# Kernel optimization log

Measured on AMD Instinct MI355X. Metric: run time of the kernel, lower is better.

Reference implementation:

```python
import jax, jax.numpy as jnp
import numpy as np

L = 256
C = 20
B = 4096


def _pairwise_mask(L, C):
    # mask[l1, c1, l2, c2] = (l2 - l1 >= 1), independent of c1, c2
    ls = np.arange(L)
    m = (ls[None, :] - ls[:, None]) >= 1            # (L, L)
    mask = np.broadcast_to(m[:, None, :, None], (L, C, L, C))
    return jnp.asarray(mask[None], dtype=bool)       # (1, L, C, L, C)


def setup_inputs() -> dict:
    key = jax.random.key(0)
    k1, k2, k3, k4 = jax.random.split(key, 4)
    # one-hot sequences, flattened to (B, L*C) like the layer's input
    seq = jax.random.randint(k1, (B, L), 0, C)
    x_lc = jax.nn.one_hot(seq, C, dtype=jnp.float32).reshape(B, L * C)
    theta_0 = jax.random.normal(k2, (1,), dtype=jnp.float32)
    theta_lc = (jax.random.normal(k3, (1, L, C), dtype=jnp.float32)
                / np.sqrt(L).astype(np.float32))
    mask = _pairwise_mask(L, C)
    theta_lclc = (jax.random.normal(k4, (1, L, C, L, C), dtype=jnp.float32)
                  / np.float32(L)) * mask
    return {"x_lc": x_lc, "theta_0": theta_0, "theta_lc": theta_lc,
            "theta_lclc": theta_lclc, "mask": mask}


def reference(x_lc, theta_0, theta_lc, theta_lclc, mask):
    # x_lc: (B, L*C); reshape to (B, L, C)
    x = x_lc.reshape(-1, L, C)
    # additive term: sum over (l, c)
    phi = theta_0 + jnp.einsum('blc,lc->b', x, theta_lc[0])[:, None]  # (B, 1)
    # masked pairwise quadratic form: x^T (theta * mask) x, computed as a
    # GEMM instead of materializing the (B, L, C, L, C) broadcast tensor.
    Theta = (theta_lclc[0] * mask[0].astype(theta_lclc.dtype)).reshape(L * C, L * C)
    xf = x_lc  # (B, L*C)
    quad = jnp.sum((xf @ Theta) * xf, axis=1, keepdims=True)  # (B, 1)
    return phi + quad
```

## Files before the change

### kernel.cpp

```cpp
#include <hip/hip_runtime.h>

#define LPOS 256
#define CCH 20
#define BB 4096
#define LC 5120


__global__ __launch_bounds__(256) void k_prepare(
    const float* __restrict__ x_lc, const float* __restrict__ theta_0,
    const float* __restrict__ theta_lc, unsigned char* __restrict__ seqC,
    float* __restrict__ out)
{
    const int b = blockIdx.x;
    const int l = threadIdx.x;
    const float* xp = x_lc + (size_t)b * LC + (size_t)l * CCH;
    const float4* xp4 = reinterpret_cast<const float4*>(xp);
    float v[CCH];
#pragma unroll
    for (int q = 0; q < 5; ++q) {
        float4 t = xp4[q];
        v[q * 4 + 0] = t.x; v[q * 4 + 1] = t.y;
        v[q * 4 + 2] = t.z; v[q * 4 + 3] = t.w;
    }
    int s = 0; float best = v[0];
#pragma unroll
    for (int c = 1; c < CCH; ++c) { if (v[c] > best) { best = v[c]; s = c; } }

    seqC[((size_t)(l >> 3) * BB + b) * 8 + (l & 7)] = (unsigned char)s;

    float lin = theta_lc[l * CCH + s];
#pragma unroll
    for (int off = 32; off > 0; off >>= 1) lin += __shfl_down(lin, off, 64);
    __shared__ float partial[4];
    const int wave = threadIdx.x >> 6;
    const int lane = threadIdx.x & 63;
    if (lane == 0) partial[wave] = lin;
    __syncthreads();
    if (threadIdx.x == 0)
        out[b] = theta_0[0] + partial[0] + partial[1] + partial[2] + partial[3];
}

#define QT 512
#define NC 8
#define NMC 32
#define NQUADS 800
#define SEGS 13
#define TBLP (SEGS * 256)

template <int MODE>
__global__ __launch_bounds__(QT, 8) void k_quad(
    const float* __restrict__ Theta,
    const uint2* __restrict__ seqC,
    float* __restrict__ part,
    float* __restrict__ out)
{
    __shared__ float Tl[TBLP];

    const int c   = blockIdx.x;
    const int g   = blockIdx.y;
    const int tid = threadIdx.x;
    const int wave = tid >> 6;
    const int lane = tid & 63;

    const int l1arr[2] = { g, 254 - g };
    const int m0a = (g + 1) >> 3;
    const int m0b = (255 - g) >> 3;
    const int n1 = NMC - m0a;
    const int L  = (g == 127) ? n1 : n1 + (NMC - m0b);

    int base[2][8];
#pragma unroll
    for (int q = 0; q < 2; ++q) {
        const int l1 = l1arr[q];
        const int mw = l1 >> 3;
        const int wsel = (l1 >> 2) & 1;
        const int sh = (l1 & 3) * 8;
#pragma unroll
        for (int i = 0; i < 8; ++i) {
            const uint2 u = seqC[(size_t)mw * BB + i * QT + tid];
            const unsigned w = wsel ? u.y : u.x;
            base[q][i] = (int)((w >> sh) & 0xFFu) * CCH;
        }
    }

    float acc[8];
#pragma unroll
    for (int i = 0; i < 8; ++i) acc[i] = 0.f;

    for (int t = c; t < L; t += NC) {
        int l1, m, jl, rq;
        if (t < n1) { rq = 0; l1 = l1arr[0]; m = m0a + t;
                      jl = (t == 0) ? ((l1 + 1) & 7) : 0; }
        else        { rq = 1; l1 = l1arr[1]; m = m0b + (t - n1);
                      jl = (t == n1) ? ((l1 + 1) & 7) : 0; }

        __syncthreads();
#pragma unroll
        for (int k = 0; k < 2; ++k) {
            const int seg = wave + 8 * k;
            if (seg < SEGS) {
                const int u0 = seg * 64 + lane;
                const int u = (u0 < NQUADS) ? u0 : (NQUADS - 1);
                const int r = u / 5, cc = u - r * 5;
                const int j = r / CCH, s1 = r - j * CCH;
                const float* gp = Theta + (size_t)(l1 * CCH + s1) * LC
                                        + (m * 8 + j) * CCH + cc * 4;
                float* lp = Tl + seg * 256;
                __builtin_amdgcn_global_load_lds(
                    (const __attribute__((address_space(1))) void*)gp,
                    (__attribute__((address_space(3))) void*)lp, 16, 0, 0);
            }
        }
        __syncthreads();

        if (jl == 0) {
#pragma unroll
            for (int i = 0; i < 8; ++i) {
                const uint2 u = seqC[(size_t)m * BB + i * QT + tid];
#pragma unroll
                for (int j = 0; j < 8; ++j) {
                    const unsigned w = (j < 4) ? u.x : u.y;
                    const int s2 = (w >> ((j & 3) * 8)) & 0xFF;
                    acc[i] += Tl[j * 400 + base[rq][i] + s2];
                }
            }
        } else {
#pragma unroll
            for (int i = 0; i < 8; ++i) {
                const uint2 u = seqC[(size_t)m * BB + i * QT + tid];
#pragma unroll
                for (int j = 0; j < 8; ++j) {
                    const unsigned w = (j < 4) ? u.x : u.y;
                    const int s2 = (w >> ((j & 3) * 8)) & 0xFF;
                    const float v = Tl[j * 400 + base[rq][i] + s2];
                    acc[i] += (j >= jl) ? v : 0.f;
                }
            }
        }
    }

    if (MODE == 0) {
        float* row = part + (size_t)(c * 128 + g) * BB;
#pragma unroll
        for (int i = 0; i < 8; ++i) row[i * QT + tid] = acc[i];
    } else {
#pragma unroll
        for (int i = 0; i < 8; ++i) atomicAdd(&out[i * QT + tid], acc[i]);
    }
}

__global__ __launch_bounds__(256) void k_reduce(
    const float4* __restrict__ part4,
    float* __restrict__ out)
{
    const int b4 = blockIdx.x * 256 + threadIdx.x;
    const int r0 = blockIdx.y * 128;
    float4 a = make_float4(0.f, 0.f, 0.f, 0.f);
    for (int r = r0; r < r0 + 128; ++r) {
        const float4 p = part4[(size_t)r * 1024 + b4];
        a.x += p.x; a.y += p.y; a.z += p.z; a.w += p.w;
    }
    atomicAdd(&out[b4 * 4 + 0], a.x);
    atomicAdd(&out[b4 * 4 + 1], a.y);
    atomicAdd(&out[b4 * 4 + 2], a.z);
    atomicAdd(&out[b4 * 4 + 3], a.w);
}

extern "C" void kernel_launch(void* const* d_in, const int* in_sizes, int n_in,
                              void* d_out, int out_size, void* d_ws, size_t ws_size,
                              hipStream_t stream) {
    const float* x_lc       = (const float*)d_in[0];
    const float* theta_0    = (const float*)d_in[1];
    const float* theta_lc   = (const float*)d_in[2];
    const float* theta_lclc = (const float*)d_in[3];
    float* out = (float*)d_out;

    unsigned char* seqC = (unsigned char*)d_ws;
    float* part = (float*)((char*)d_ws + (1 << 20));
    const size_t need = (1 << 20) + (size_t)1024 * BB * 4;

    k_prepare<<<dim3(BB), dim3(256), 0, stream>>>(x_lc, theta_0, theta_lc, seqC, out);
    if (ws_size >= need) {
        k_quad<0><<<dim3(NC, 128), dim3(QT), 0, stream>>>(
            theta_lclc, (const uint2*)seqC, part, out);
        k_reduce<<<dim3(4, 8), dim3(256), 0, stream>>>(
            (const float4*)part, out);
    } else {
        k_quad<1><<<dim3(NC, 128), dim3(QT), 0, stream>>>(
            theta_lclc, (const uint2*)seqC, part, out);
    }
}
```

Baseline: 68.80 us.

## Flatten quad work into 4-chunk blocks with double-buffered LDS staging

Replaces the 8x128 grid, where each block walks a strided list of (l1, m) chunks, with a flat grid of 1048 blocks that each process four consecutive chunks. Theta tiles are double-buffered in LDS so the next chunk's global_load_lds runs while the current one is consumed. The sequence words and base indices for the next chunk are prefetched into registers. This doubles LDS use per block, which may lower occupancy, and grows the partial buffer and reduction to 1048 rows.

After: 248.9 us. 262% more time.

```diff
diff --git a/kernel.cpp b/kernel.cpp
--- a/kernel.cpp
+++ b/kernel.cpp
@@ -41,11 +41,12 @@
 }
 
 #define QT 512
-#define NC 8
 #define NMC 32
 #define NQUADS 800
 #define SEGS 13
 #define TBLP (SEGS * 256)
+#define NCHT 4192
+#define NBLK (NCHT / 4)
 
 template <int MODE>
 __global__ __launch_bounds__(QT, 8) void k_quad(
@@ -54,47 +55,32 @@
     float* __restrict__ part,
     float* __restrict__ out)
 {
-    __shared__ float Tl[TBLP];
-
-    const int c   = blockIdx.x;
-    const int g   = blockIdx.y;
+    __shared__ float Tl[2 * TBLP];
+
+    const int blk = blockIdx.x;
     const int tid = threadIdx.x;
     const int wave = tid >> 6;
     const int lane = tid & 63;
 
-    const int l1arr[2] = { g, 254 - g };
-    const int m0a = (g + 1) >> 3;
-    const int m0b = (255 - g) >> 3;
-    const int n1 = NMC - m0a;
-    const int L  = (g == 127) ? n1 : n1 + (NMC - m0b);
-
-    int base[2][8];
-#pragma unroll
-    for (int q = 0; q < 2; ++q) {
-        const int l1 = l1arr[q];
-        const int mw = l1 >> 3;
-        const int wsel = (l1 >> 2) & 1;
-        const int sh = (l1 & 3) * 8;
-#pragma unroll
-        for (int i = 0; i < 8; ++i) {
-            const uint2 u = seqC[(size_t)mw * BB + i * QT + tid];
-            const unsigned w = wsel ? u.y : u.x;
-            base[q][i] = (int)((w >> sh) & 0xFFu) * CCH;
-        }
-    }
-
-    float acc[8];
-#pragma unroll
-    for (int i = 0; i < 8; ++i) acc[i] = 0.f;
-
-    for (int t = c; t < L; t += NC) {
-        int l1, m, jl, rq;
-        if (t < n1) { rq = 0; l1 = l1arr[0]; m = m0a + t;
-                      jl = (t == 0) ? ((l1 + 1) & 7) : 0; }
-        else        { rq = 1; l1 = l1arr[1]; m = m0b + (t - n1);
-                      jl = (t == n1) ? ((l1 + 1) & 7) : 0; }
-
-        __syncthreads();
+    int cl1[4], cm[4], cjl[4];
+    {
+        int T = blk * 4, l1 = 0;
+        for (; l1 < 255; ++l1) {
+            const int cnt = NMC - ((l1 + 1) >> 3);
+            if (T < cnt) break;
+            T -= cnt;
+        }
+        int m = ((l1 + 1) >> 3) + T;
+#pragma unroll
+        for (int d = 0; d < 4; ++d) {
+            cl1[d] = l1; cm[d] = m;
+            cjl[d] = (m == ((l1 + 1) >> 3)) ? ((l1 + 1) & 7) : 0;
+            ++m;
+            if (m == NMC) { ++l1; m = (l1 + 1) >> 3; }
+        }
+    }
+
+    auto stage = [&](int l1, int m, int dst) {
 #pragma unroll
         for (int k = 0; k < 2; ++k) {
             const int seg = wave + 8 * k;
@@ -105,42 +91,79 @@
                 const int j = r / CCH, s1 = r - j * CCH;
                 const float* gp = Theta + (size_t)(l1 * CCH + s1) * LC
                                         + (m * 8 + j) * CCH + cc * 4;
-                float* lp = Tl + seg * 256;
+                float* lp = Tl + dst * TBLP + seg * 256;
                 __builtin_amdgcn_global_load_lds(
                     (const __attribute__((address_space(1))) void*)gp,
                     (__attribute__((address_space(3))) void*)lp, 16, 0, 0);
             }
         }
-        __syncthreads();
-
+    };
+    auto loadbase = [&](int l1, int* basev) {
+        const int mw = l1 >> 3;
+        const int wsel = (l1 >> 2) & 1;
+        const int sh = (l1 & 3) * 8;
+#pragma unroll
+        for (int i = 0; i < 8; ++i) {
+            const uint2 u = seqC[(size_t)mw * BB + i * QT + tid];
+            const unsigned w = wsel ? u.y : u.x;
+            basev[i] = (int)((w >> sh) & 0xFFu) * CCH;
+        }
+    };
+
+    float acc[8];
+#pragma unroll
+    for (int i = 0; i < 8; ++i) acc[i] = 0.f;
+
+    int basev[8];
+    uint2 squ[8];
+
+    stage(cl1[0], cm[0], 0);
+    loadbase(cl1[0], basev);
+#pragma unroll
+    for (int i = 0; i < 8; ++i)
+        squ[i] = seqC[(size_t)cm[0] * BB + i * QT + tid];
+    __syncthreads();
+
+#pragma unroll
+    for (int d = 0; d < 4; ++d) {
+        if (d < 3) stage(cl1[d + 1], cm[d + 1], (d + 1) & 1);
+        const float* T = Tl + (d & 1) * TBLP;
+        const int jl = cjl[d];
         if (jl == 0) {
 #pragma unroll
             for (int i = 0; i < 8; ++i) {
-                const uint2 u = seqC[(size_t)m * BB + i * QT + tid];
+                const uint2 u = squ[i];
 #pragma unroll
                 for (int j = 0; j < 8; ++j) {
                     const unsigned w = (j < 4) ? u.x : u.y;
                     const int s2 = (w >> ((j & 3) * 8)) & 0xFF;
-                    acc[i] += Tl[j * 400 + base[rq][i] + s2];
+                    acc[i] += T[j * 400 + basev[i] + s2];
                 }
             }
         } else {
 #pragma unroll
             for (int i = 0; i < 8; ++i) {
-                const uint2 u = seqC[(size_t)m * BB + i * QT + tid];
+                const uint2 u = squ[i];
 #pragma unroll
                 for (int j = 0; j < 8; ++j) {
                     const unsigned w = (j < 4) ? u.x : u.y;
                     const int s2 = (w >> ((j & 3) * 8)) & 0xFF;
-                    const float v = Tl[j * 400 + base[rq][i] + s2];
+                    const float v = T[j * 400 + basev[i] + s2];
                     acc[i] += (j >= jl) ? v : 0.f;
                 }
             }
         }
+        if (d < 3) {
+            if (cl1[d + 1] != cl1[d]) loadbase(cl1[d + 1], basev);
+#pragma unroll
+            for (int i = 0; i < 8; ++i)
+                squ[i] = seqC[(size_t)cm[d + 1] * BB + i * QT + tid];
+        }
+        __syncthreads();
     }
 
     if (MODE == 0) {
-        float* row = part + (size_t)(c * 128 + g) * BB;
+        float* row = part + (size_t)blk * BB;
 #pragma unroll
         for (int i = 0; i < 8; ++i) row[i * QT + tid] = acc[i];
     } else {
@@ -154,9 +177,10 @@
     float* __restrict__ out)
 {
     const int b4 = blockIdx.x * 256 + threadIdx.x;
-    const int r0 = blockIdx.y * 128;
+    const int r0 = blockIdx.y * 131;
+    const int r1 = min(r0 + 131, NBLK);
     float4 a = make_float4(0.f, 0.f, 0.f, 0.f);
-    for (int r = r0; r < r0 + 128; ++r) {
+    for (int r = r0; r < r1; ++r) {
         const float4 p = part4[(size_t)r * 1024 + b4];
         a.x += p.x; a.y += p.y; a.z += p.z; a.w += p.w;
     }
@@ -177,16 +201,16 @@
 
     unsigned char* seqC = (unsigned char*)d_ws;
     float* part = (float*)((char*)d_ws + (1 << 20));
-    const size_t need = (1 << 20) + (size_t)1024 * BB * 4;
+    const size_t need = (1 << 20) + (size_t)NBLK * BB * 4;
 
     k_prepare<<<dim3(BB), dim3(256), 0, stream>>>(x_lc, theta_0, theta_lc, seqC, out);
     if (ws_size >= need) {
-        k_quad<0><<<dim3(NC, 128), dim3(QT), 0, stream>>>(
+        k_quad<0><<<dim3(NBLK), dim3(QT), 0, stream>>>(
             theta_lclc, (const uint2*)seqC, part, out);
         k_reduce<<<dim3(4, 8), dim3(256), 0, stream>>>(
             (const float4*)part, out);
     } else {
-        k_quad<1><<<dim3(NC, 128), dim3(QT), 0, stream>>>(
+        k_quad<1><<<dim3(NBLK), dim3(QT), 0, stream>>>(
             theta_lclc, (const uint2*)seqC, part, out);
     }
 }
```
